# Kernel tuning notes

Hardware: AMD Instinct MI355X
Metric: run time of the kernel (lower is better)

## Reference

```python
import jax, jax.numpy as jnp
import numpy as np

MAPSIZE = 256          # nearest power of two >= 224
BITS = 8               # log2(MAPSIZE)
PAD = (MAPSIZE - 224) // 2  # 16
WIBBLEDECAY = 2.0
EPSILON = 0.128
GREY = jnp.array([0.485, 0.45, 0.406], dtype=jnp.float32)


def fog_creator(fog_vars, bsize, mapsize, wibbledecay):
    """Diamond-square fractal noise with learnable perturbations (faithful port)."""
    m = jnp.zeros((bsize, mapsize, mapsize), dtype=jnp.float32)
    step = mapsize
    wibble = 1.0
    v = 0
    while step >= 2:
        h = step // 2
        # --- fillsquares: square centers = mean of 4 corners + wibble ---
        corner = m[:, 0:mapsize:step, 0:mapsize:step]          # (B, g, g)
        acc = corner + jnp.roll(corner, -1, axis=1)
        acc = acc + jnp.roll(acc, -1, axis=2)
        m = m.at[:, h:mapsize:step, h:mapsize:step].set(acc / 4.0 + wibble * fog_vars[v])
        v += 1
        # --- filldiamonds: diamond centers = mean of 4 neighbors + wibble ---
        dr = m[:, h:mapsize:step, h:mapsize:step]
        ul = m[:, 0:mapsize:step, 0:mapsize:step]
        lt = (dr + jnp.roll(dr, 1, axis=1)) + (ul + jnp.roll(ul, -1, axis=2))
        tt = (dr + jnp.roll(dr, 1, axis=2)) + (ul + jnp.roll(ul, -1, axis=1))
        m = m.at[:, 0:mapsize:step, h:mapsize:step].set(lt / 4.0 + wibble * fog_vars[v])
        v += 1
        m = m.at[:, h:mapsize:step, 0:mapsize:step].set(tt / 4.0 + wibble * fog_vars[v])
        v += 1
        step //= 2
        wibble /= wibbledecay
    return jnp.clip(jnp.abs(m), 0.0, 1.0)[:, None, :, :]  # (B, 1, M, M)


def apply_fog(inputs, fog):
    return inputs * (1.0 - fog) + fog * GREY.reshape(1, 3, 1, 1)


def setup_inputs() -> dict:
    key = jax.random.key(0)
    B = 256
    keys = jax.random.split(key, 3 * BITS + 1)
    inp = {"inputs": jax.random.uniform(keys[0], (B, 3, 224, 224), dtype=jnp.float32)}
    k = 1
    for i in range(BITS):
        g = 2 ** i
        for j in range(3):
            name = f"fog_{3 * i + j:02d}"
            inp[name] = EPSILON * jax.random.uniform(keys[k], (B, g, g), dtype=jnp.float32)
            k += 1
    return inp


def reference(inputs, fog_00, fog_01, fog_02, fog_03, fog_04, fog_05, fog_06, fog_07,
              fog_08, fog_09, fog_10, fog_11, fog_12, fog_13, fog_14, fog_15, fog_16,
              fog_17, fog_18, fog_19, fog_20, fog_21, fog_22, fog_23):
    fog_vars = [fog_00, fog_01, fog_02, fog_03, fog_04, fog_05, fog_06, fog_07,
                fog_08, fog_09, fog_10, fog_11, fog_12, fog_13, fog_14, fog_15,
                fog_16, fog_17, fog_18, fog_19, fog_20, fog_21, fog_22, fog_23]
    fog = fog_creator(fog_vars, inputs.shape[0], MAPSIZE, WIBBLEDECAY)
    fog = fog[:, :, PAD:-PAD, PAD:-PAD]  # crop 256 -> 224
    return apply_fog(inputs, fog)
```

## Files before the change

kernel.cpp:

```cpp
#include <hip/hip_runtime.h>


#define MAPB 128

struct FogPtrs { const float* f[24]; };

__global__ __launch_bounds__(1024) void fog_coarse(FogPtrs fp, float* __restrict__ Cout) {
    __shared__ float Bm[MAPB * MAPB];
    const int b = blockIdx.x;
    const int t = threadIdx.x;
    if (t == 0) Bm[0] = 0.0f;
    __syncthreads();
    float w = 1.0f;
    for (int k = 0; k < 7; ++k) {
        const int n = 1 << k, mask = n - 1;
        const int S = MAPB >> k, H = S >> 1;
        const int nn = n * n;
        const float* __restrict__ f0 = fp.f[3 * k]     + b * nn;
        const float* __restrict__ f1 = fp.f[3 * k + 1] + b * nn;
        const float* __restrict__ f2 = fp.f[3 * k + 2] + b * nn;
        for (int idx = t; idx < nn; idx += 1024) {
            const int i = idx >> k, j = idx & mask;
            const int i1 = (i + 1) & mask, j1 = (j + 1) & mask;
            const float c00 = Bm[i  * S * MAPB + j  * S];
            const float c10 = Bm[i1 * S * MAPB + j  * S];
            const float c01 = Bm[i  * S * MAPB + j1 * S];
            const float c11 = Bm[i1 * S * MAPB + j1 * S];
            Bm[(i * S + H) * MAPB + j * S + H] = (c00 + c10 + c01 + c11) * 0.25f + w * f0[idx];
        }
        __syncthreads();
        for (int idx = t; idx < nn; idx += 1024) {
            const int i = idx >> k, j = idx & mask;
            const int i1 = (i + 1) & mask, j1 = (j + 1) & mask;
            const int im = (i - 1) & mask, jm = (j - 1) & mask;
            const float dij = Bm[(i  * S + H) * MAPB + j  * S + H];
            const float dmi = Bm[(im * S + H) * MAPB + j  * S + H];
            const float dmj = Bm[(i  * S + H) * MAPB + jm * S + H];
            const float c00 = Bm[i  * S * MAPB + j  * S];
            const float c01 = Bm[i  * S * MAPB + j1 * S];
            const float c10 = Bm[i1 * S * MAPB + j  * S];
            Bm[i * S * MAPB + j * S + H]       = (dij + dmi + c00 + c01) * 0.25f + w * f1[idx];
            Bm[(i * S + H) * MAPB + j * S]     = (dij + dmj + c00 + c10) * 0.25f + w * f2[idx];
        }
        __syncthreads();
        w *= 0.5f;
    }
    float4* __restrict__ dst = (float4*)(Cout + (size_t)b * (MAPB * MAPB));
    const float4* src = (const float4*)Bm;
    for (int idx = t; idx < MAPB * MAPB / 4; idx += 1024) dst[idx] = src[idx];
}

__global__ __launch_bounds__(256) void fog_apply(
    const float* __restrict__ inp,
    const float* __restrict__ Cg,
    const float* __restrict__ f21, const float* __restrict__ f22, const float* __restrict__ f23,
    float* __restrict__ out)
{
    __shared__ float sC[18 * 128];
    __shared__ float sD[17 * 128];
    const int b  = blockIdx.y;
    const int r0 = blockIdx.x * 32;
    const int t  = threadIdx.x;
    const int ci0 = (r0 >> 1) + 7;

    const float* __restrict__ Cb = Cg + (size_t)b * 16384 + ci0 * 128;
    for (int idx = t; idx < 18 * 128; idx += 256) sC[idx] = Cb[idx];
    __syncthreads();

    const float w7 = 0.0078125f;
    const float* __restrict__ f21b = f21 + (size_t)b * 16384 + ci0 * 128;
    for (int idx = t; idx < 17 * 128; idx += 256) {
        const int di = idx >> 7, j = idx & 127;
        const int j1 = (j + 1) & 127;
        sD[idx] = (sC[di * 128 + j] + sC[(di + 1) * 128 + j] +
                   sC[di * 128 + j1] + sC[(di + 1) * 128 + j1]) * 0.25f
                  + w7 * f21b[idx];
    }
    __syncthreads();

    const float* __restrict__ f22b = f22 + (size_t)b * 16384;
    const float* __restrict__ f23b = f23 + (size_t)b * 16384;
    for (int q = t; q < 16 * 112; q += 256) {
        const int qr = q / 112;
        const int qc = q - qr * 112;
        const int di = qr + 1;
        const int j  = qc + 8;
        const int gi = ci0 + di;
        const float c00 = sC[di * 128 + j];
        const float d11 = sD[di * 128 + j];
        const float mlt = (d11 + sD[(di - 1) * 128 + j] + c00 + sC[di * 128 + j + 1]) * 0.25f
                          + w7 * f22b[gi * 128 + j];
        const float mtt = (d11 + sD[di * 128 + j - 1] + c00 + sC[(di + 1) * 128 + j]) * 0.25f
                          + w7 * f23b[gi * 128 + j];
        const float f00 = fminf(fabsf(c00), 1.0f);
        const float f01 = fminf(fabsf(mlt), 1.0f);
        const float f10 = fminf(fabsf(mtt), 1.0f);
        const float f11 = fminf(fabsf(d11), 1.0f);

        const int row0 = r0 + 2 * qr;
        const int col  = 2 * qc;
        #pragma unroll
        for (int ch = 0; ch < 3; ++ch) {
            const float g = (ch == 0) ? 0.485f : ((ch == 1) ? 0.45f : 0.406f);
            const size_t base = ((size_t)(b * 3 + ch) * 224 + row0) * 224 + col;
            const float2 x0 = *(const float2*)(inp + base);
            const float2 x1 = *(const float2*)(inp + base + 224);
            float2 o0, o1;
            o0.x = x0.x * (1.0f - f00) + f00 * g;
            o0.y = x0.y * (1.0f - f01) + f01 * g;
            o1.x = x1.x * (1.0f - f10) + f10 * g;
            o1.y = x1.y * (1.0f - f11) + f11 * g;
            *(float2*)(out + base)       = o0;
            *(float2*)(out + base + 224) = o1;
        }
    }
}

extern "C" void kernel_launch(void* const* d_in, const int* in_sizes, int n_in,
                              void* d_out, int out_size, void* d_ws, size_t ws_size,
                              hipStream_t stream) {
    (void)in_sizes; (void)n_in; (void)out_size; (void)ws_size;
    const float* inp = (const float*)d_in[0];
    FogPtrs fp;
    for (int v = 0; v < 24; ++v) fp.f[v] = (const float*)d_in[1 + v];
    float* Cg = (float*)d_ws;

    fog_coarse<<<dim3(256), dim3(1024), 0, stream>>>(fp, Cg);
    fog_apply<<<dim3(7, 256), dim3(256), 0, stream>>>(
        inp, Cg, fp.f[21], fp.f[22], fp.f[23], (float*)d_out);
}
```

Measured before the change: 359.6 us.

## Prefetch fog perturbations into registers and widen fog_apply tiles with float4 I/O

In fog_coarse, all per-level perturbation values (levels 0-6) are loaded into registers up front so global-load latency is paid once rather than serialized between barriers, and the last coarse level is fully unrolled. fog_apply now processes 56 output rows per block with 512 threads and computes four output columns per thread, so input/output traffic uses float4 accesses and the halo recomputation per block shrinks. This adds register pressure and fewer blocks (4x256) in exchange for wider memory transactions.

```diff
diff --git a/kernel.cpp b/kernel.cpp
--- a/kernel.cpp
+++ b/kernel.cpp
@@ -9,28 +9,50 @@
     __shared__ float Bm[MAPB * MAPB];
     const int b = blockIdx.x;
     const int t = threadIdx.x;
+
+    float pf0[6], pf1[6], pf2[6];
+    #pragma unroll
+    for (int k = 0; k < 6; ++k) {
+        const int nn = 1 << (2 * k);
+        if (t < nn) {
+            pf0[k] = fp.f[3 * k]    [(size_t)b * nn + t];
+            pf1[k] = fp.f[3 * k + 1][(size_t)b * nn + t];
+            pf2[k] = fp.f[3 * k + 2][(size_t)b * nn + t];
+        }
+    }
+    float q0[4], q1[4], q2[4];
+    {
+        const float* __restrict__ f0 = fp.f[18] + (size_t)b * 4096;
+        const float* __restrict__ f1 = fp.f[19] + (size_t)b * 4096;
+        const float* __restrict__ f2 = fp.f[20] + (size_t)b * 4096;
+        #pragma unroll
+        for (int it = 0; it < 4; ++it) {
+            q0[it] = f0[t + it * 1024];
+            q1[it] = f1[t + it * 1024];
+            q2[it] = f2[t + it * 1024];
+        }
+    }
     if (t == 0) Bm[0] = 0.0f;
     __syncthreads();
+
     float w = 1.0f;
-    for (int k = 0; k < 7; ++k) {
+    #pragma unroll
+    for (int k = 0; k < 6; ++k) {
         const int n = 1 << k, mask = n - 1;
         const int S = MAPB >> k, H = S >> 1;
         const int nn = n * n;
-        const float* __restrict__ f0 = fp.f[3 * k]     + b * nn;
-        const float* __restrict__ f1 = fp.f[3 * k + 1] + b * nn;
-        const float* __restrict__ f2 = fp.f[3 * k + 2] + b * nn;
-        for (int idx = t; idx < nn; idx += 1024) {
-            const int i = idx >> k, j = idx & mask;
+        if (t < nn) {
+            const int i = t >> k, j = t & mask;
             const int i1 = (i + 1) & mask, j1 = (j + 1) & mask;
             const float c00 = Bm[i  * S * MAPB + j  * S];
             const float c10 = Bm[i1 * S * MAPB + j  * S];
             const float c01 = Bm[i  * S * MAPB + j1 * S];
             const float c11 = Bm[i1 * S * MAPB + j1 * S];
-            Bm[(i * S + H) * MAPB + j * S + H] = (c00 + c10 + c01 + c11) * 0.25f + w * f0[idx];
-        }
-        __syncthreads();
-        for (int idx = t; idx < nn; idx += 1024) {
-            const int i = idx >> k, j = idx & mask;
+            Bm[(i * S + H) * MAPB + j * S + H] = (c00 + c10 + c01 + c11) * 0.25f + w * pf0[k];
+        }
+        __syncthreads();
+        if (t < nn) {
+            const int i = t >> k, j = t & mask;
             const int i1 = (i + 1) & mask, j1 = (j + 1) & mask;
             const int im = (i - 1) & mask, jm = (j - 1) & mask;
             const float dij = Bm[(i  * S + H) * MAPB + j  * S + H];
@@ -39,37 +61,71 @@
             const float c00 = Bm[i  * S * MAPB + j  * S];
             const float c01 = Bm[i  * S * MAPB + j1 * S];
             const float c10 = Bm[i1 * S * MAPB + j  * S];
-            Bm[i * S * MAPB + j * S + H]       = (dij + dmi + c00 + c01) * 0.25f + w * f1[idx];
-            Bm[(i * S + H) * MAPB + j * S]     = (dij + dmj + c00 + c10) * 0.25f + w * f2[idx];
+            Bm[i * S * MAPB + j * S + H]   = (dij + dmi + c00 + c01) * 0.25f + w * pf1[k];
+            Bm[(i * S + H) * MAPB + j * S] = (dij + dmj + c00 + c10) * 0.25f + w * pf2[k];
         }
         __syncthreads();
         w *= 0.5f;
+    }
+    {
+        const float w6 = 0.015625f;
+        #pragma unroll
+        for (int it = 0; it < 4; ++it) {
+            const int idx = t + it * 1024;
+            const int i = idx >> 6, j = idx & 63;
+            const int i1 = (i + 1) & 63, j1 = (j + 1) & 63;
+            const float c00 = Bm[i  * 2 * MAPB + j  * 2];
+            const float c10 = Bm[i1 * 2 * MAPB + j  * 2];
+            const float c01 = Bm[i  * 2 * MAPB + j1 * 2];
+            const float c11 = Bm[i1 * 2 * MAPB + j1 * 2];
+            Bm[(i * 2 + 1) * MAPB + j * 2 + 1] = (c00 + c10 + c01 + c11) * 0.25f + w6 * q0[it];
+        }
+        __syncthreads();
+        #pragma unroll
+        for (int it = 0; it < 4; ++it) {
+            const int idx = t + it * 1024;
+            const int i = idx >> 6, j = idx & 63;
+            const int i1 = (i + 1) & 63, j1 = (j + 1) & 63;
+            const int im = (i - 1) & 63, jm = (j - 1) & 63;
+            const float dij = Bm[(i  * 2 + 1) * MAPB + j  * 2 + 1];
+            const float dmi = Bm[(im * 2 + 1) * MAPB + j  * 2 + 1];
+            const float dmj = Bm[(i  * 2 + 1) * MAPB + jm * 2 + 1];
+            const float c00 = Bm[i  * 2 * MAPB + j  * 2];
+            const float c01 = Bm[i  * 2 * MAPB + j1 * 2];
+            const float c10 = Bm[i1 * 2 * MAPB + j  * 2];
+            Bm[i * 2 * MAPB + j * 2 + 1]   = (dij + dmi + c00 + c01) * 0.25f + w6 * q1[it];
+            Bm[(i * 2 + 1) * MAPB + j * 2] = (dij + dmj + c00 + c10) * 0.25f + w6 * q2[it];
+        }
+        __syncthreads();
     }
     float4* __restrict__ dst = (float4*)(Cout + (size_t)b * (MAPB * MAPB));
     const float4* src = (const float4*)Bm;
-    for (int idx = t; idx < MAPB * MAPB / 4; idx += 1024) dst[idx] = src[idx];
+    #pragma unroll
+    for (int it = 0; it < 4; ++it) dst[t + it * 1024] = src[t + it * 1024];
 }
 
-__global__ __launch_bounds__(256) void fog_apply(
+__global__ __launch_bounds__(512) void fog_apply(
     const float* __restrict__ inp,
     const float* __restrict__ Cg,
     const float* __restrict__ f21, const float* __restrict__ f22, const float* __restrict__ f23,
     float* __restrict__ out)
 {
-    __shared__ float sC[18 * 128];
-    __shared__ float sD[17 * 128];
+    __shared__ __align__(16) float sC[30 * 128];
+    __shared__ __align__(16) float sD[29 * 128];
     const int b  = blockIdx.y;
-    const int r0 = blockIdx.x * 32;
+    const int r0 = blockIdx.x * 56;
     const int t  = threadIdx.x;
     const int ci0 = (r0 >> 1) + 7;
 
-    const float* __restrict__ Cb = Cg + (size_t)b * 16384 + ci0 * 128;
-    for (int idx = t; idx < 18 * 128; idx += 256) sC[idx] = Cb[idx];
+    const float4* __restrict__ Cb4 = (const float4*)(Cg + (size_t)b * 16384 + (size_t)ci0 * 128);
+    float4* __restrict__ sC4 = (float4*)sC;
+    sC4[t] = Cb4[t];
+    if (t < 448) sC4[t + 512] = Cb4[t + 512];
     __syncthreads();
 
     const float w7 = 0.0078125f;
-    const float* __restrict__ f21b = f21 + (size_t)b * 16384 + ci0 * 128;
-    for (int idx = t; idx < 17 * 128; idx += 256) {
+    const float* __restrict__ f21b = f21 + (size_t)b * 16384 + (size_t)ci0 * 128;
+    for (int idx = t; idx < 29 * 128; idx += 512) {
         const int di = idx >> 7, j = idx & 127;
         const int j1 = (j + 1) & 127;
         sD[idx] = (sC[di * 128 + j] + sC[(di + 1) * 128 + j] +
@@ -80,38 +136,56 @@
 
     const float* __restrict__ f22b = f22 + (size_t)b * 16384;
     const float* __restrict__ f23b = f23 + (size_t)b * 16384;
-    for (int q = t; q < 16 * 112; q += 256) {
-        const int qr = q / 112;
-        const int qc = q - qr * 112;
-        const int di = qr + 1;
-        const int j  = qc + 8;
+    for (int p = t; p < 28 * 56; p += 512) {
+        const int pr = p / 56;
+        const int pc = p - pr * 56;
+        const int di = pr + 1;
+        const int j0 = 2 * pc + 8;
         const int gi = ci0 + di;
-        const float c00 = sC[di * 128 + j];
-        const float d11 = sD[di * 128 + j];
-        const float mlt = (d11 + sD[(di - 1) * 128 + j] + c00 + sC[di * 128 + j + 1]) * 0.25f
-                          + w7 * f22b[gi * 128 + j];
-        const float mtt = (d11 + sD[di * 128 + j - 1] + c00 + sC[(di + 1) * 128 + j]) * 0.25f
-                          + w7 * f23b[gi * 128 + j];
-        const float f00 = fminf(fabsf(c00), 1.0f);
-        const float f01 = fminf(fabsf(mlt), 1.0f);
-        const float f10 = fminf(fabsf(mtt), 1.0f);
-        const float f11 = fminf(fabsf(d11), 1.0f);
-
-        const int row0 = r0 + 2 * qr;
-        const int col  = 2 * qc;
+        const float c0  = sC[di * 128 + j0];
+        const float c1  = sC[di * 128 + j0 + 1];
+        const float c2  = sC[di * 128 + j0 + 2];
+        const float cb0 = sC[(di + 1) * 128 + j0];
+        const float cb1 = sC[(di + 1) * 128 + j0 + 1];
+        const float dm  = sD[di * 128 + j0 - 1];
+        const float d0  = sD[di * 128 + j0];
+        const float d1  = sD[di * 128 + j0 + 1];
+        const float du0 = sD[(di - 1) * 128 + j0];
+        const float du1 = sD[(di - 1) * 128 + j0 + 1];
+        const float2 v22 = *(const float2*)(f22b + (size_t)gi * 128 + j0);
+        const float2 v23 = *(const float2*)(f23b + (size_t)gi * 128 + j0);
+        const float lt0 = (d0 + du0 + c0 + c1) * 0.25f + w7 * v22.x;
+        const float lt1 = (d1 + du1 + c1 + c2) * 0.25f + w7 * v22.y;
+        const float tt0 = (d0 + dm + c0 + cb0) * 0.25f + w7 * v23.x;
+        const float tt1 = (d1 + d0 + c1 + cb1) * 0.25f + w7 * v23.y;
+        const float fa = fminf(fabsf(c0),  1.0f);
+        const float fb = fminf(fabsf(lt0), 1.0f);
+        const float fc = fminf(fabsf(c1),  1.0f);
+        const float fd = fminf(fabsf(lt1), 1.0f);
+        const float fe = fminf(fabsf(tt0), 1.0f);
+        const float ff = fminf(fabsf(d0),  1.0f);
+        const float fg = fminf(fabsf(tt1), 1.0f);
+        const float fh = fminf(fabsf(d1),  1.0f);
+
+        const int orow = r0 + 2 * pr;
+        const int ocol = 4 * pc;
         #pragma unroll
         for (int ch = 0; ch < 3; ++ch) {
             const float g = (ch == 0) ? 0.485f : ((ch == 1) ? 0.45f : 0.406f);
-            const size_t base = ((size_t)(b * 3 + ch) * 224 + row0) * 224 + col;
-            const float2 x0 = *(const float2*)(inp + base);
-            const float2 x1 = *(const float2*)(inp + base + 224);
-            float2 o0, o1;
-            o0.x = x0.x * (1.0f - f00) + f00 * g;
-            o0.y = x0.y * (1.0f - f01) + f01 * g;
-            o1.x = x1.x * (1.0f - f10) + f10 * g;
-            o1.y = x1.y * (1.0f - f11) + f11 * g;
-            *(float2*)(out + base)       = o0;
-            *(float2*)(out + base + 224) = o1;
+            const size_t base = ((size_t)(b * 3 + ch) * 224 + orow) * 224 + ocol;
+            const float4 x0 = *(const float4*)(inp + base);
+            const float4 x1 = *(const float4*)(inp + base + 224);
+            float4 o0, o1;
+            o0.x = x0.x * (1.0f - fa) + fa * g;
+            o0.y = x0.y * (1.0f - fb) + fb * g;
+            o0.z = x0.z * (1.0f - fc) + fc * g;
+            o0.w = x0.w * (1.0f - fd) + fd * g;
+            o1.x = x1.x * (1.0f - fe) + fe * g;
+            o1.y = x1.y * (1.0f - ff) + ff * g;
+            o1.z = x1.z * (1.0f - fg) + fg * g;
+            o1.w = x1.w * (1.0f - fh) + fh * g;
+            *(float4*)(out + base)       = o0;
+            *(float4*)(out + base + 224) = o1;
         }
     }
 }
@@ -126,6 +200,6 @@
     float* Cg = (float*)d_ws;
 
     fog_coarse<<<dim3(256), dim3(1024), 0, stream>>>(fp, Cg);
-    fog_apply<<<dim3(7, 256), dim3(256), 0, stream>>>(
+    fog_apply<<<dim3(4, 256), dim3(512), 0, stream>>>(
         inp, Cg, fp.f[21], fp.f[22], fp.f[23], (float*)d_out);
 }
```

After: 355.1 us. About the same (-1.2%).
